# Optimization experiments

Measured on AMD Instinct MI355X. Metric: run time of the kernel, lower is better.

## Reference

```python
import jax, jax.numpy as jnp
import numpy as np

D_MODEL = 1024
N_HEADS = 16
HEAD_DIM = D_MODEL // N_HEADS


def setup_inputs() -> dict:
    key = jax.random.key(0)
    ks = jax.random.split(key, 11)
    B, S = 8, 1024
    scale = 1.0 / np.sqrt(D_MODEL)
    inp = {
        "query": jax.random.normal(ks[0], (B, S, D_MODEL), jnp.float32),
        "key": jax.random.normal(ks[1], (B, S, D_MODEL), jnp.float32),
        "value": jax.random.normal(ks[2], (B, S, D_MODEL), jnp.float32),
        "Wq": jax.random.normal(ks[3], (D_MODEL, D_MODEL), jnp.float32) * scale,
        "bq": jnp.zeros((D_MODEL,), jnp.float32),
        "Wk": jax.random.normal(ks[4], (D_MODEL, D_MODEL), jnp.float32) * scale,
        "bk": jnp.zeros((D_MODEL,), jnp.float32),
        "Wv": jax.random.normal(ks[5], (D_MODEL, D_MODEL), jnp.float32) * scale,
        "bv": jnp.zeros((D_MODEL,), jnp.float32),
        "Wo": jax.random.normal(ks[6], (D_MODEL, D_MODEL), jnp.float32) * scale,
        "bo": jnp.zeros((D_MODEL,), jnp.float32),
    }
    return inp


def reference(query, key, value, Wq, bq, Wk, bk, Wv, bv, Wo, bo):
    B, S, _ = query.shape
    # projections (torch Linear: x @ W.T + b)
    Q = query @ Wq.T + bq
    K = key @ Wk.T + bk
    V = value @ Wv.T + bv
    # [B, H, S, Dh]
    Q = Q.reshape(B, S, N_HEADS, HEAD_DIM).transpose(0, 2, 1, 3)
    K = K.reshape(B, S, N_HEADS, HEAD_DIM).transpose(0, 2, 1, 3)
    V = V.reshape(B, S, N_HEADS, HEAD_DIM).transpose(0, 2, 1, 3)
    scores = jnp.einsum("bhqd,bhkd->bhqk", Q, K) / np.sqrt(HEAD_DIM).astype(np.float32)
    attention = jax.nn.softmax(scores, axis=-1)
    context = jnp.einsum("bhqk,bhkd->bhqd", attention, V)
    context = context.transpose(0, 2, 1, 3).reshape(B, S, D_MODEL)
    output = context @ Wo.T + bo
    return output, attention
```

## Files before the change

### kernel.cpp

```cpp
#include <hip/hip_runtime.h>
#include <cstddef>

typedef _Float16 f16;
typedef f16 f16x8 __attribute__((ext_vector_type(8)));
typedef short s16x8 __attribute__((ext_vector_type(8)));
typedef short s16x4 __attribute__((ext_vector_type(4)));
typedef float f32x4 __attribute__((ext_vector_type(4)));

#define S_LEN 1024
#define NH 16
#define HD 64
#define MROWS 8192
#define WPLANE 1048576

__device__ __forceinline__ f32x4 mfma_f16(f16x8 a, f16x8 b, f32x4 c) {
  return __builtin_amdgcn_mfma_f32_16x16x32_f16(a, b, c, 0, 0, 0);
}
__device__ __forceinline__ short f2h(float x) {
  f16 h = (f16)x;
  return __builtin_bit_cast(short, h);
}
__device__ __forceinline__ float h2f(short s) {
  return (float)__builtin_bit_cast(f16, s);
}

typedef const __attribute__((address_space(1))) unsigned int* as1_u32p;
typedef __attribute__((address_space(3))) unsigned int* as3_u32p;
__device__ __forceinline__ void gl_lds16(const short* g, short* l) {
  __builtin_amdgcn_global_load_lds((as1_u32p)(const void*)g,
                                   (as3_u32p)(void*)l, 16, 0, 0);
}

__global__ __launch_bounds__(256) void convw4_k(
    const float* __restrict__ W0, const float* __restrict__ W1,
    const float* __restrict__ W2, const float* __restrict__ W3,
    short* __restrict__ out) {
  const int wsel = blockIdx.y;
  const float* W = wsel == 0 ? W0 : (wsel == 1 ? W1 : (wsel == 2 ? W2 : W3));
  const int i = (blockIdx.x * 256 + threadIdx.x) * 8;
  const int n = i >> 10, kg = i & 1023;
  const int dst = (((n >> 7) * 32 + (kg >> 5)) * 128 + (n & 127)) * 32 + (kg & 31);
  float xs[8];
  *(float4*)&xs[0] = *(const float4*)&W[i];
  *(float4*)&xs[4] = *(const float4*)&W[i + 4];
  s16x8 H;
#pragma unroll
  for (int j = 0; j < 8; ++j) H[j] = f2h(xs[j]);
  *(s16x8*)&out[(size_t)wsel * WPLANE + dst] = H;
}

__global__ __launch_bounds__(256, 2) void qkvproj_k(
    const float* __restrict__ Aq, const float* __restrict__ Ak,
    const float* __restrict__ Av, const short* __restrict__ Wpl,
    const float* __restrict__ bq, const float* __restrict__ bk,
    const float* __restrict__ bv, short* __restrict__ Oq,
    short* __restrict__ Ok, short* __restrict__ Ovt) {
  __shared__ __align__(16) short Ah[128][40];
  __shared__ __align__(16) short Bh[128][32];
  const int pid = blockIdx.y;
  const float* Af = pid == 0 ? Aq : (pid == 1 ? Ak : Av);
  const float* bias = pid == 0 ? bq : (pid == 1 ? bk : bv);
  const short* Whi = Wpl + (size_t)pid * WPLANE;

  const int t = threadIdx.x, lane = t & 63, wid = t >> 6;
  const int wr = wid >> 1, wc = wid & 1;
  const int fr = lane & 15, fg = lane >> 4;
  const int bid = blockIdx.x;
  const int wg = (bid & 7) * 64 + (bid >> 3);
  const int bm = (wg >> 3) * 128, bn = (wg & 7) * 128;
  const int srow = t >> 1, sk = (t & 1) * 16;

  f32x4 acc[4][4] = {};

  for (int ks = 0; ks < 32; ++ks) {
    const int k0 = ks * 32;
    {
      const size_t boff = ((size_t)(bn >> 7) * 32 + ks) * 4096;
      const int c0 = wid * 2;
      gl_lds16(&Whi[boff + (size_t)c0 * 512 + lane * 8],       &Bh[0][0] + c0 * 512);
      gl_lds16(&Whi[boff + (size_t)(c0 + 1) * 512 + lane * 8], &Bh[0][0] + (c0 + 1) * 512);
    }
    {
      const float* ap = &Af[(size_t)(bm + srow) * 1024 + k0 + sk];
      float xs[16];
      *(float4*)&xs[0]  = *(const float4*)(ap);
      *(float4*)&xs[4]  = *(const float4*)(ap + 4);
      *(float4*)&xs[8]  = *(const float4*)(ap + 8);
      *(float4*)&xs[12] = *(const float4*)(ap + 12);
      s16x8 H0, H1;
#pragma unroll
      for (int j = 0; j < 8; ++j) { H0[j] = f2h(xs[j]); H1[j] = f2h(xs[8 + j]); }
      *(s16x8*)&Ah[srow][sk] = H0; *(s16x8*)&Ah[srow][sk + 8] = H1;
    }
    __syncthreads();
    f16x8 ah[4], bh[4];
#pragma unroll
    for (int f = 0; f < 4; ++f) {
      ah[f] = *(const f16x8*)&Ah[wr * 64 + f * 16 + fr][fg * 8];
      bh[f] = *(const f16x8*)&Bh[wc * 64 + f * 16 + fr][fg * 8];
    }
#pragma unroll
    for (int i = 0; i < 4; ++i)
#pragma unroll
      for (int j = 0; j < 4; ++j)
        acc[i][j] = mfma_f16(ah[i], bh[j], acc[i][j]);
    __syncthreads();
  }

#pragma unroll
  for (int i = 0; i < 4; ++i) {
#pragma unroll
    for (int j = 0; j < 4; ++j) {
      const int m0 = bm + wr * 64 + i * 16 + fg * 4;
      const int n  = bn + wc * 64 + j * 16 + fr;
      const float bb = bias[n];
      const int batch = m0 >> 10, s0 = m0 & 1023;
      const int h = n >> 6, d = n & 63;
      if (pid < 2) {
        short* O = pid == 0 ? Oq : Ok;
        const size_t base = ((size_t)(batch * NH + h) * S_LEN + s0) * HD + d;
#pragma unroll
        for (int r = 0; r < 4; ++r)
          O[base + (size_t)r * HD] = f2h(acc[i][j][r] + bb);
      } else {
        s16x4 pk;
#pragma unroll
        for (int r = 0; r < 4; ++r) pk[r] = f2h(acc[i][j][r] + bb);
        *(s16x4*)&Ovt[((size_t)(batch * NH + h) * HD + d) * S_LEN + s0] = pk;
      }
    }
  }
}

__global__ __launch_bounds__(256, 2) void oproj_k(
    const short* __restrict__ Ahi, const short* __restrict__ Whi,
    const float* __restrict__ bias, float* __restrict__ Of) {
  __shared__ __align__(16) short Ah[128][32];
  __shared__ __align__(16) short Bh[128][32];
  const int t = threadIdx.x, lane = t & 63, wid = t >> 6;
  const int wr = wid >> 1, wc = wid & 1;
  const int fr = lane & 15, fg = lane >> 4;
  const int bid = blockIdx.x;
  const int wg = (bid & 7) * 64 + (bid >> 3);
  const int bm = (wg >> 3) * 128, bn = (wg & 7) * 128;

  f32x4 acc[4][4] = {};

  for (int ks = 0; ks < 32; ++ks) {
    {
      const size_t boff = ((size_t)(bn >> 7) * 32 + ks) * 4096;
      const size_t aoff = ((size_t)(bm >> 7) * 32 + ks) * 4096;
      const int c0 = wid * 2;
      gl_lds16(&Whi[boff + (size_t)c0 * 512 + lane * 8],       &Bh[0][0] + c0 * 512);
      gl_lds16(&Whi[boff + (size_t)(c0 + 1) * 512 + lane * 8], &Bh[0][0] + (c0 + 1) * 512);
      gl_lds16(&Ahi[aoff + (size_t)c0 * 512 + lane * 8],       &Ah[0][0] + c0 * 512);
      gl_lds16(&Ahi[aoff + (size_t)(c0 + 1) * 512 + lane * 8], &Ah[0][0] + (c0 + 1) * 512);
    }
    __syncthreads();
    f16x8 ah[4], bh[4];
#pragma unroll
    for (int f = 0; f < 4; ++f) {
      ah[f] = *(const f16x8*)&Ah[wr * 64 + f * 16 + fr][fg * 8];
      bh[f] = *(const f16x8*)&Bh[wc * 64 + f * 16 + fr][fg * 8];
    }
#pragma unroll
    for (int i = 0; i < 4; ++i)
#pragma unroll
      for (int j = 0; j < 4; ++j)
        acc[i][j] = mfma_f16(ah[i], bh[j], acc[i][j]);
    __syncthreads();
  }

#pragma unroll
  for (int i = 0; i < 4; ++i) {
#pragma unroll
    for (int j = 0; j < 4; ++j) {
      const int m0 = bm + wr * 64 + i * 16 + fg * 4;
      const int n  = bn + wc * 64 + j * 16 + fr;
      const float bb = bias[n];
#pragma unroll
      for (int r = 0; r < 4; ++r)
        Of[(size_t)(m0 + r) * 1024 + n] = acc[i][j][r] + bb;
    }
  }
}

template <bool FUSE_PV>
__global__ __launch_bounds__(512) void attn_k(
    const short* __restrict__ Qp, const short* __restrict__ Kp,
    const short* __restrict__ Vt, float* __restrict__ attn,
    short* __restrict__ Cp) {
  __shared__ __align__(16) short Kh[64][72];
  __shared__ __align__(16) short Vs[FUSE_PV ? 64 : 1][72];
  __shared__ __align__(16) short Pt[FUSE_PV ? 128 : 1][72];
  __shared__ float sums[2][128];
  __shared__ float sinv[128];

  const int wg = blockIdx.x;
  const int w  = (wg & 7) * 128 + (wg >> 3);
  const int bh = w >> 3;
  const int qb = (w & 7) * 128;
  const int batch = bh >> 4, h = bh & 15;

  const int t = threadIdx.x, lane = t & 63, wid = t >> 6;
  const int wq = wid >> 1, wk = wid & 1;
  const int fr = lane & 15, fg = lane >> 4;
  const int srow = t >> 3, sc = (t & 7) * 8;

  f16x8 qh[2][2];
#pragma unroll
  for (int fm = 0; fm < 2; ++fm)
#pragma unroll
    for (int kc = 0; kc < 2; ++kc) {
      const size_t qa =
          ((size_t)bh * S_LEN + qb + wq * 32 + fm * 16 + fr) * HD + kc * 32 + fg * 8;
      qh[fm][kc] = *(const f16x8*)&Qp[qa];
    }

  float rs[2] = {};
  for (int kt = 0; kt < 16; ++kt) {
    const size_t kb = ((size_t)bh * S_LEN + kt * 64 + srow) * HD + sc;
    *(s16x8*)&Kh[srow][sc] = *(const s16x8*)&Kp[kb];
    __syncthreads();
    f16x8 kh[2][2];
#pragma unroll
    for (int fn = 0; fn < 2; ++fn)
#pragma unroll
      for (int kc = 0; kc < 2; ++kc)
        kh[fn][kc] = *(const f16x8*)&Kh[wk * 32 + fn * 16 + fr][kc * 32 + fg * 8];
    f32x4 s4[2][2] = {};
#pragma unroll
    for (int fn = 0; fn < 2; ++fn)
#pragma unroll
      for (int fm = 0; fm < 2; ++fm)
#pragma unroll
        for (int kc = 0; kc < 2; ++kc)
          s4[fn][fm] = mfma_f16(kh[fn][kc], qh[fm][kc], s4[fn][fm]);
#pragma unroll
    for (int fn = 0; fn < 2; ++fn)
#pragma unroll
      for (int fm = 0; fm < 2; ++fm)
#pragma unroll
        for (int r = 0; r < 4; ++r)
          rs[fm] += __expf(s4[fn][fm][r] * 0.125f);
    __syncthreads();
  }
#pragma unroll
  for (int fm = 0; fm < 2; ++fm) {
    float v = rs[fm];
    v += __shfl_xor(v, 16); v += __shfl_xor(v, 32);
    if (fg == 0) sums[wk][wq * 32 + fm * 16 + fr] = v;
  }
  __syncthreads();
  if (t < 128) sinv[t] = 1.0f / (sums[0][t] + sums[1][t]);
  __syncthreads();

  float pinv[2];
#pragma unroll
  for (int fm = 0; fm < 2; ++fm) pinv[fm] = sinv[wq * 32 + fm * 16 + fr];

  f32x4 apv[2][2] = {};
  for (int kt = 0; kt < 16; ++kt) {
    {
      const size_t kb = ((size_t)bh * S_LEN + kt * 64 + srow) * HD + sc;
      *(s16x8*)&Kh[srow][sc] = *(const s16x8*)&Kp[kb];
      if constexpr (FUSE_PV) {
        const short* vrow = Vt + ((size_t)bh * HD + srow) * S_LEN + kt * 64 + sc;
        *(s16x8*)&Vs[srow][sc] = *(const s16x8*)(vrow);
      }
    }
    __syncthreads();
    f16x8 kh[2][2];
#pragma unroll
    for (int fn = 0; fn < 2; ++fn)
#pragma unroll
      for (int kc = 0; kc < 2; ++kc)
        kh[fn][kc] = *(const f16x8*)&Kh[wk * 32 + fn * 16 + fr][kc * 32 + fg * 8];
    f32x4 s4[2][2] = {};
#pragma unroll
    for (int fn = 0; fn < 2; ++fn)
#pragma unroll
      for (int fm = 0; fm < 2; ++fm)
#pragma unroll
        for (int kc = 0; kc < 2; ++kc)
          s4[fn][fm] = mfma_f16(kh[fn][kc], qh[fm][kc], s4[fn][fm]);
#pragma unroll
    for (int fm = 0; fm < 2; ++fm) {
#pragma unroll
      for (int fn = 0; fn < 2; ++fn) {
        const int kbase = wk * 32 + fn * 16 + fg * 4;
        if constexpr (FUSE_PV) {
          s16x4 pk;
#pragma unroll
          for (int r = 0; r < 4; ++r)
            pk[r] = f2h(__expf(s4[fn][fm][r] * 0.125f) * pinv[fm]);
          *(s16x4*)&Pt[wq * 32 + fm * 16 + fr][kbase] = pk;
        } else {
          const int q = qb + wq * 32 + fm * 16 + fr;
          float4 e4;
          e4.x = __expf(s4[fn][fm][0] * 0.125f) * pinv[fm];
          e4.y = __expf(s4[fn][fm][1] * 0.125f) * pinv[fm];
          e4.z = __expf(s4[fn][fm][2] * 0.125f) * pinv[fm];
          e4.w = __expf(s4[fn][fm][3] * 0.125f) * pinv[fm];
          *(float4*)&attn[((size_t)bh * S_LEN + q) * S_LEN + kt * 64 + kbase] = e4;
        }
      }
    }
    __syncthreads();
    if constexpr (FUSE_PV) {
      {
        const int r0 = t >> 4, c4 = (t & 15) * 4;
#pragma unroll
        for (int it = 0; it < 4; ++it) {
          const int q = r0 + it * 32;
          const s16x4 p4 = *(const s16x4*)&Pt[q][c4];
          float4 o;
          o.x = h2f(p4[0]); o.y = h2f(p4[1]);
          o.z = h2f(p4[2]); o.w = h2f(p4[3]);
          *(float4*)&attn[((size_t)bh * S_LEN + qb + q) * S_LEN + kt * 64 + c4] = o;
        }
      }
      f16x8 af[2][2], bv[2][2];
#pragma unroll
      for (int f = 0; f < 2; ++f)
#pragma unroll
        for (int kc = 0; kc < 2; ++kc) {
          af[f][kc] = *(const f16x8*)&Pt[wq * 32 + f * 16 + fr][kc * 32 + fg * 8];
          bv[f][kc] = *(const f16x8*)&Vs[wk * 32 + f * 16 + fr][kc * 32 + fg * 8];
        }
#pragma unroll
      for (int i = 0; i < 2; ++i)
#pragma unroll
        for (int j = 0; j < 2; ++j)
#pragma unroll
          for (int kc = 0; kc < 2; ++kc)
            apv[i][j] = mfma_f16(af[i][kc], bv[j][kc], apv[i][j]);
      __syncthreads();
    }
  }

  if constexpr (FUSE_PV) {
#pragma unroll
    for (int i = 0; i < 2; ++i)
#pragma unroll
      for (int j = 0; j < 2; ++j) {
        const int s0 = qb + wq * 32 + i * 16 + fg * 4;
        const int d = h * HD + wk * 32 + j * 16 + fr;
#pragma unroll
        for (int r = 0; r < 4; ++r) {
          const int m = batch * S_LEN + s0 + r;
          const size_t idx =
              (((size_t)(m >> 7) * 32 + (d >> 5)) * 128 + (m & 127)) * 32 + (d & 31);
          Cp[idx] = f2h(apv[i][j][r]);
        }
      }
  }
}

__global__ __launch_bounds__(256) void pv2_k(
    const float* __restrict__ attn, const short* __restrict__ Vt,
    short* __restrict__ Cp) {
  __shared__ __align__(16) short At[64][72], Vs[64][72];
  const int wg = blockIdx.x;
  const int w  = (wg & 7) * 256 + (wg >> 3);
  const int bh = w >> 4;
  const int qb = (w & 15) * 64;
  const int batch = bh >> 4, h = bh & 15;
  const int t = threadIdx.x, lane = t & 63, wid = t >> 6;
  const int wq = wid >> 1, wd = wid & 1;
  const int fr = lane & 15, fg = lane >> 4;
  const int srow = t >> 2, sc = (t & 3) * 16;
  const float* arow = attn + ((size_t)bh * S_LEN + qb + srow) * S_LEN + sc;
  const short* vrow = Vt + ((size_t)bh * HD + srow) * S_LEN + sc;

  f32x4 acc[2][2] = {};
  for (int kt = 0; kt < 16; ++kt) {
    float xs[16];
    *(float4*)&xs[0]  = *(const float4*)(arow + kt * 64);
    *(float4*)&xs[4]  = *(const float4*)(arow + kt * 64 + 4);
    *(float4*)&xs[8]  = *(const float4*)(arow + kt * 64 + 8);
    *(float4*)&xs[12] = *(const float4*)(arow + kt * 64 + 12);
    s16x8 c0, c1;
#pragma unroll
    for (int j = 0; j < 8; ++j) { c0[j] = f2h(xs[j]); c1[j] = f2h(xs[8 + j]); }
    const s16x8 v0 = *(const s16x8*)(vrow + kt * 64);
    const s16x8 v1 = *(const s16x8*)(vrow + kt * 64 + 8);
    *(s16x8*)&At[srow][sc] = c0; *(s16x8*)&At[srow][sc + 8] = c1;
    *(s16x8*)&Vs[srow][sc] = v0; *(s16x8*)&Vs[srow][sc + 8] = v1;
    __syncthreads();
    f16x8 af[2][2], bv[2][2];
#pragma unroll
    for (int f = 0; f < 2; ++f)
#pragma unroll
      for (int kc = 0; kc < 2; ++kc) {
        af[f][kc] = *(const f16x8*)&At[wq * 32 + f * 16 + fr][kc * 32 + fg * 8];
        bv[f][kc] = *(const f16x8*)&Vs[wd * 32 + f * 16 + fr][kc * 32 + fg * 8];
      }
#pragma unroll
    for (int i = 0; i < 2; ++i)
#pragma unroll
      for (int j = 0; j < 2; ++j)
#pragma unroll
        for (int kc = 0; kc < 2; ++kc)
          acc[i][j] = mfma_f16(af[i][kc], bv[j][kc], acc[i][j]);
    __syncthreads();
  }

#pragma unroll
  for (int i = 0; i < 2; ++i)
#pragma unroll
    for (int j = 0; j < 2; ++j) {
      const int s0 = qb + wq * 32 + i * 16 + fg * 4;
      const int d = h * HD + wd * 32 + j * 16 + fr;
#pragma unroll
      for (int r = 0; r < 4; ++r) {
        const int m = batch * S_LEN + s0 + r;
        const size_t idx =
            (((size_t)(m >> 7) * 32 + (d >> 5)) * 128 + (m & 127)) * 32 + (d & 31);
        Cp[idx] = f2h(acc[i][j][r]);
      }
    }
}

extern "C" void kernel_launch(void* const* d_in, const int* in_sizes, int n_in,
                              void* d_out, int out_size, void* d_ws, size_t ws_size,
                              hipStream_t stream) {
  const float* query = (const float*)d_in[0];
  const float* key   = (const float*)d_in[1];
  const float* value = (const float*)d_in[2];
  const float* Wq    = (const float*)d_in[3];
  const float* bq    = (const float*)d_in[4];
  const float* Wk    = (const float*)d_in[5];
  const float* bk    = (const float*)d_in[6];
  const float* Wv    = (const float*)d_in[7];
  const float* bv    = (const float*)d_in[8];
  const float* Wo    = (const float*)d_in[9];
  const float* bo    = (const float*)d_in[10];

  float* out  = (float*)d_out;
  float* attn = out + (size_t)MROWS * 1024;

  short* qp = (short*)d_ws;
  short* kp = qp + 8388608;
  short* vt = kp + 8388608;
  short* w4 = vt + 8388608;
  short* cx = w4 + 4 * WPLANE;

  const size_t need_fused = ((size_t)4 * 8388608 + 4 * WPLANE) * sizeof(short);
  const bool fuse = ws_size >= need_fused;

  const dim3 blk(256);

  convw4_k<<<dim3(512, 4), blk, 0, stream>>>(Wq, Wk, Wv, Wo, w4);
  qkvproj_k<<<dim3(512, 3), blk, 0, stream>>>(query, key, value, w4,
                                              bq, bk, bv, qp, kp, vt);

  short* ctxPlane;
  if (fuse) {
    attn_k<true><<<dim3(1024), dim3(512), 0, stream>>>(qp, kp, vt, attn, cx);
    ctxPlane = cx;
  } else {
    attn_k<false><<<dim3(1024), dim3(512), 0, stream>>>(qp, kp, vt, attn, nullptr);
    pv2_k<<<dim3(2048), blk, 0, stream>>>(attn, vt, qp);
    ctxPlane = qp;
  }

  oproj_k<<<dim3(512), blk, 0, stream>>>(ctxPlane, w4 + 3 * WPLANE, bo, out);
}
```

Baseline: 380.0 us.

## Pre-convert activations to tiled fp16 and stream them via global_load_lds

Adds a separate conversion kernel that writes query/key/value as fp16 in a tiled, GEMM-ready layout. The QKV projection then loads A tiles straight into LDS with global_load_lds instead of doing fp32 loads and fp16 conversion in-loop, and raises launch bounds occupancy to 4 blocks per SM. The workspace is reorganised so the fused attention path always runs, with the context buffer reusing the third activation plane. This costs an extra pass over the activations (fp32 read plus fp16 write) and assumes the workspace is large enough, since the non-fused fallback is removed.

```diff
diff --git a/kernel.cpp b/kernel.cpp
--- a/kernel.cpp
+++ b/kernel.cpp
@@ -12,6 +12,7 @@
 #define HD 64
 #define MROWS 8192
 #define WPLANE 1048576
+#define APLANE 8388608
 
 __device__ __forceinline__ f32x4 mfma_f16(f16x8 a, f16x8 b, f32x4 c) {
   return __builtin_amdgcn_mfma_f32_16x16x32_f16(a, b, c, 0, 0, 0);
@@ -49,17 +50,33 @@
   *(s16x8*)&out[(size_t)wsel * WPLANE + dst] = H;
 }
 
-__global__ __launch_bounds__(256, 2) void qkvproj_k(
-    const float* __restrict__ Aq, const float* __restrict__ Ak,
-    const float* __restrict__ Av, const short* __restrict__ Wpl,
+__global__ __launch_bounds__(256) void conva_k(
+    const float* __restrict__ A0, const float* __restrict__ A1,
+    const float* __restrict__ A2, short* __restrict__ out) {
+  const int asel = blockIdx.y;
+  const float* A = asel == 0 ? A0 : (asel == 1 ? A1 : A2);
+  const int i = (blockIdx.x * 256 + threadIdx.x) * 8;
+  const int m = i >> 10, kg = i & 1023;
+  const int dst = (((m >> 7) * 32 + (kg >> 5)) * 128 + (m & 127)) * 32 + (kg & 31);
+  float xs[8];
+  *(float4*)&xs[0] = *(const float4*)&A[i];
+  *(float4*)&xs[4] = *(const float4*)&A[i + 4];
+  s16x8 H;
+#pragma unroll
+  for (int j = 0; j < 8; ++j) H[j] = f2h(xs[j]);
+  *(s16x8*)&out[(size_t)asel * APLANE + dst] = H;
+}
+
+__global__ __launch_bounds__(256, 4) void qkvproj_k(
+    const short* __restrict__ Apl, const short* __restrict__ Wpl,
     const float* __restrict__ bq, const float* __restrict__ bk,
     const float* __restrict__ bv, short* __restrict__ Oq,
     short* __restrict__ Ok, short* __restrict__ Ovt) {
-  __shared__ __align__(16) short Ah[128][40];
+  __shared__ __align__(16) short Ah[128][32];
   __shared__ __align__(16) short Bh[128][32];
   const int pid = blockIdx.y;
-  const float* Af = pid == 0 ? Aq : (pid == 1 ? Ak : Av);
   const float* bias = pid == 0 ? bq : (pid == 1 ? bk : bv);
+  const short* Ahi = Apl + (size_t)pid * APLANE;
   const short* Whi = Wpl + (size_t)pid * WPLANE;
 
   const int t = threadIdx.x, lane = t & 63, wid = t >> 6;
@@ -68,29 +85,18 @@
   const int bid = blockIdx.x;
   const int wg = (bid & 7) * 64 + (bid >> 3);
   const int bm = (wg >> 3) * 128, bn = (wg & 7) * 128;
-  const int srow = t >> 1, sk = (t & 1) * 16;
 
   f32x4 acc[4][4] = {};
 
   for (int ks = 0; ks < 32; ++ks) {
-    const int k0 = ks * 32;
     {
       const size_t boff = ((size_t)(bn >> 7) * 32 + ks) * 4096;
+      const size_t aoff = ((size_t)(bm >> 7) * 32 + ks) * 4096;
       const int c0 = wid * 2;
       gl_lds16(&Whi[boff + (size_t)c0 * 512 + lane * 8],       &Bh[0][0] + c0 * 512);
       gl_lds16(&Whi[boff + (size_t)(c0 + 1) * 512 + lane * 8], &Bh[0][0] + (c0 + 1) * 512);
-    }
-    {
-      const float* ap = &Af[(size_t)(bm + srow) * 1024 + k0 + sk];
-      float xs[16];
-      *(float4*)&xs[0]  = *(const float4*)(ap);
-      *(float4*)&xs[4]  = *(const float4*)(ap + 4);
-      *(float4*)&xs[8]  = *(const float4*)(ap + 8);
-      *(float4*)&xs[12] = *(const float4*)(ap + 12);
-      s16x8 H0, H1;
-#pragma unroll
-      for (int j = 0; j < 8; ++j) { H0[j] = f2h(xs[j]); H1[j] = f2h(xs[8 + j]); }
-      *(s16x8*)&Ah[srow][sk] = H0; *(s16x8*)&Ah[srow][sk + 8] = H1;
+      gl_lds16(&Ahi[aoff + (size_t)c0 * 512 + lane * 8],       &Ah[0][0] + c0 * 512);
+      gl_lds16(&Ahi[aoff + (size_t)(c0 + 1) * 512 + lane * 8], &Ah[0][0] + (c0 + 1) * 512);
     }
     __syncthreads();
     f16x8 ah[4], bh[4];
@@ -440,30 +446,20 @@
   float* out  = (float*)d_out;
   float* attn = out + (size_t)MROWS * 1024;
 
-  short* qp = (short*)d_ws;
-  short* kp = qp + 8388608;
-  short* vt = kp + 8388608;
-  short* w4 = vt + 8388608;
-  short* cx = w4 + 4 * WPLANE;
-
-  const size_t need_fused = ((size_t)4 * 8388608 + 4 * WPLANE) * sizeof(short);
-  const bool fuse = ws_size >= need_fused;
+  short* apl = (short*)d_ws;
+  short* qp  = apl + 3 * (size_t)APLANE;
+  short* kp  = qp + APLANE;
+  short* vt  = kp + APLANE;
+  short* w4  = vt + APLANE;
+  short* cx  = apl + 2 * (size_t)APLANE;
 
   const dim3 blk(256);
 
   convw4_k<<<dim3(512, 4), blk, 0, stream>>>(Wq, Wk, Wv, Wo, w4);
-  qkvproj_k<<<dim3(512, 3), blk, 0, stream>>>(query, key, value, w4,
-                                              bq, bk, bv, qp, kp, vt);
-
-  short* ctxPlane;
-  if (fuse) {
-    attn_k<true><<<dim3(1024), dim3(512), 0, stream>>>(qp, kp, vt, attn, cx);
-    ctxPlane = cx;
-  } else {
-    attn_k<false><<<dim3(1024), dim3(512), 0, stream>>>(qp, kp, vt, attn, nullptr);
-    pv2_k<<<dim3(2048), blk, 0, stream>>>(attn, vt, qp);
-    ctxPlane = qp;
-  }
-
-  oproj_k<<<dim3(512), blk, 0, stream>>>(ctxPlane, w4 + 3 * WPLANE, bo, out);
-}
+  conva_k<<<dim3(4096, 3), blk, 0, stream>>>(query, key, value, apl);
+  qkvproj_k<<<dim3(512, 3), blk, 0, stream>>>(apl, w4, bq, bk, bv, qp, kp, vt);
+
+  attn_k<true><<<dim3(1024), dim3(512), 0, stream>>>(qp, kp, vt, attn, cx);
+
+  oproj_k<<<dim3(512), blk, 0, stream>>>(cx, w4 + 3 * WPLANE, bo, out);
+}
```

Result: faster. 370.8 us (-2.4%).
